# Kernel tuning notes

Hardware: AMD Instinct MI355X
Metric: run time of the kernel (lower is better)

## Reference

```python
import jax, jax.numpy as jnp
import numpy as np

B = 4096
D = 512
N_CLASSES = 100
TEMPERATURE = 0.5


def setup_inputs() -> dict:
    key = jax.random.key(0)
    k1, k2, k3 = jax.random.split(key, 3)
    emb_i = jax.random.normal(k1, (B, D), dtype=jnp.float32)
    emb_j = jax.random.normal(k2, (B, D), dtype=jnp.float32)
    target = jax.random.randint(k3, (B,), 0, N_CLASSES, dtype=jnp.int64)
    return {"emb_i": emb_i, "emb_j": emb_j, "target": target}


def _l2_normalize(x, eps=1e-12):
    # matches torch F.normalize(dim=1): x / max(||x||, eps)
    n = jnp.sqrt(jnp.sum(x * x, axis=1, keepdims=True))
    return x / jnp.maximum(n, eps)


def reference(emb_i, emb_j, target):
    size = emb_i.shape[0]          # B
    n2 = 2 * size                  # 2B
    t = jnp.float32(TEMPERATURE)

    z_i = _l2_normalize(emb_i)
    z_j = _l2_normalize(emb_j)
    reps = jnp.concatenate([z_i, z_j], axis=0)                 # [2B, D]
    sim = jnp.matmul(reps, reps.T)                             # [2B, 2B]

    # positives: diag at offsets +B and -B
    sim_ij = jnp.diagonal(sim, offset=size)                    # [B]
    sim_ji = jnp.diagonal(sim, offset=-size)                   # [B]
    positives = jnp.concatenate([sim_ij, sim_ji], axis=0)      # [2B]
    nominator = jnp.exp(positives / t)

    idx = jnp.arange(n2)
    labels = jnp.concatenate([target, target])                 # [2B]
    # sample_mask: zero where same label AND |i-j| != B (also zeros the diagonal)
    same_label = labels[:, None] == labels[None, :]
    not_pos_pair = jnp.abs(idx[:, None] - idx[None, :]) != size
    sample_mask = jnp.where(same_label & not_pos_pair, 0.0, 1.0).astype(jnp.float32)
    # negatives_mask: ~eye
    neg_mask = 1.0 - jnp.eye(n2, dtype=jnp.float32)

    denom = jnp.sum(sample_mask * neg_mask * jnp.exp(sim / t), axis=1)  # [2B]
    loss_partial = -jnp.log(nominator / (denom + 1e-7))
    loss = jnp.sum(loss_partial) / n2
    return loss
```

## Files before the change

kernel.cpp:

```cpp
#include <hip/hip_runtime.h>
#include <hip/hip_bf16.h>
#include <cstdint>

#define B_SIZE 4096
#define TWO_B  8192
#define DIM    512
#define NPAIRS 2080
#define EXP_SCALE 2.8853900817779268f

typedef __attribute__((ext_vector_type(4))) float f32x4;

#define WAITVM(n) __builtin_amdgcn_s_waitcnt(0xF70 | (n))
#define BARRIER() __builtin_amdgcn_s_barrier()

__device__ __forceinline__ void async16(const void* g, void* l) {
    __builtin_amdgcn_global_load_lds(
        (const __attribute__((address_space(1))) unsigned int*)g,
        (__attribute__((address_space(3))) unsigned int*)l,
        16, 0, 0);
}

__global__ __launch_bounds__(256) void norm_pos_kernel(
    const float* __restrict__ emb_i, const float* __restrict__ emb_j,
    unsigned char* __restrict__ reps, float* __restrict__ pos,
    float* __restrict__ denom, float* __restrict__ out)
{
    __shared__ float sc[3][4];
    int b = blockIdx.x, t = threadIdx.x;
    if (b < 32) denom[b * 256 + t] = 0.0f;
    if (b == 32 && t == 0) out[0] = 0.0f;

    const float2* ri = (const float2*)(emb_i + (size_t)b * DIM);
    const float2* rj = (const float2*)(emb_j + (size_t)b * DIM);
    float2 xi = ri[t], xj = rj[t];
    float si = xi.x * xi.x + xi.y * xi.y;
    float sj = xj.x * xj.x + xj.y * xj.y;
    #pragma unroll
    for (int o = 32; o > 0; o >>= 1) { si += __shfl_down(si, o, 64); sj += __shfl_down(sj, o, 64); }
    int lane = t & 63, w = t >> 6;
    if (lane == 0) { sc[0][w] = si; sc[1][w] = sj; }
    __syncthreads();
    float ni2 = sc[0][0] + sc[0][1] + sc[0][2] + sc[0][3];
    float nj2 = sc[1][0] + sc[1][1] + sc[1][2] + sc[1][3];
    float rni = 1.0f / fmaxf(sqrtf(ni2), 1e-12f);
    float rnj = 1.0f / fmaxf(sqrtf(nj2), 1e-12f);
    float zix = xi.x * rni, ziy = xi.y * rni;
    float zjx = xj.x * rnj, zjy = xj.y * rnj;
    int pki = __builtin_amdgcn_cvt_pk_fp8_f32(zix, ziy, 0, false);
    int pkj = __builtin_amdgcn_cvt_pk_fp8_f32(zjx, zjy, 0, false);
    ((unsigned short*)(reps + (size_t)b * DIM))[t]            = (unsigned short)pki;
    ((unsigned short*)(reps + (size_t)(b + B_SIZE) * DIM))[t] = (unsigned short)pkj;
    float d = zix * zjx + ziy * zjy;
    #pragma unroll
    for (int o = 32; o > 0; o >>= 1) d += __shfl_down(d, o, 64);
    if (lane == 0) sc[2][w] = d;
    __syncthreads();
    if (t == 0) pos[b] = sc[2][0] + sc[2][1] + sc[2][2] + sc[2][3];
}

#define BM 128
#define BK 64
#define KITERS 8

__global__ __launch_bounds__(256) void sim_denom_kernel(
    const unsigned char* __restrict__ reps,
    const int* __restrict__ target,
    float* __restrict__ denom)
{
    __shared__ __align__(16) unsigned char As0[BM * BK];
    __shared__ __align__(16) unsigned char As1[BM * BK];
    __shared__ __align__(16) unsigned char Bs0[BM * BK];
    __shared__ __align__(16) unsigned char Bs1[BM * BK];

    int t = threadIdx.x;
    int id = blockIdx.x;

    const int sI[10]  = {0,0,0,0,1,1,1,2,2,3};
    const int sJ[10]  = {0,1,2,3,1,2,3,2,3,3};
    const int off[11] = {0,136,392,648,904,1040,1296,1552,1688,1944,2080};
    int s = 0;
    while (off[s + 1] <= id) s++;
    int l = id - off[s];
    int u, v;
    if (sI[s] == sJ[s]) {
        u = 0;
        while (((u + 1) * (32 - u)) / 2 <= l) u++;
        v = u + (l - (u * (33 - u)) / 2);
    } else { u = l >> 4; v = l & 15; }
    int bi = sI[s] * 16 + u;
    int bj = sJ[s] * 16 + v;
    int brow = bi * BM;
    int bcol = bj * BM;

    int wave = t >> 6, lane = t & 63;
    int wr = wave >> 1, wc = wave & 1;
    int quad = lane >> 4, lm = lane & 15;

    f32x4 acc[4][4];
    #pragma unroll
    for (int i = 0; i < 4; i++)
        #pragma unroll
        for (int j = 0; j < 4; j++) acc[i][j] = (f32x4)0.0f;

    int srow = t >> 2;
    int sp   = (t & 3) ^ ((srow ^ (srow >> 2)) & 3);
    const unsigned char* gA = reps + (size_t)(brow + srow) * DIM + sp * 16;
    const unsigned char* gB = reps + (size_t)(bcol + srow) * DIM + sp * 16;

    auto stage = [&](unsigned char* Ab, unsigned char* Bb, int k0) {
        #pragma unroll
        for (int c = 0; c < 2; c++) {
            async16(gA + k0 + c * 64 * DIM, Ab + t * 16 + c * 4096);
            async16(gB + k0 + c * 64 * DIM, Bb + t * 16 + c * 4096);
        }
    };
    auto compute = [&](const unsigned char* Ab, const unsigned char* Bb) {
        #pragma unroll
        for (int ss = 0; ss < 2; ss++) {
            long af[4], bf[4];
            #pragma unroll
            for (int mi = 0; mi < 4; mi++) {
                int rl = wr * 64 + mi * 16 + lm;
                int p = (ss * 2 + (quad >> 1)) ^ ((rl ^ (rl >> 2)) & 3);
                af[mi] = *(const long*)(Ab + rl * 64 + p * 16 + (quad & 1) * 8);
            }
            #pragma unroll
            for (int ni = 0; ni < 4; ni++) {
                int cl = wc * 64 + ni * 16 + lm;
                int p = (ss * 2 + (quad >> 1)) ^ ((cl ^ (cl >> 2)) & 3);
                bf[ni] = *(const long*)(Bb + cl * 64 + p * 16 + (quad & 1) * 8);
            }
            #pragma unroll
            for (int mi = 0; mi < 4; mi++)
                #pragma unroll
                for (int ni = 0; ni < 4; ni++)
                    acc[mi][ni] = __builtin_amdgcn_mfma_f32_16x16x32_fp8_fp8(
                        af[mi], bf[ni], acc[mi][ni], 0, 0, 0);
        }
    };

    stage(As0, Bs0, 0);
    stage(As1, Bs1, BK);

    #pragma unroll
    for (int k = 0; k < KITERS; k++) {
        unsigned char* Ac = (k & 1) ? As1 : As0;
        unsigned char* Bc = (k & 1) ? Bs1 : Bs0;
        if (k < KITERS - 1) WAITVM(4); else WAITVM(0);
        BARRIER();
        compute(Ac, Bc);
        BARRIER();
        if (k + 2 < KITERS) stage(Ac, Bc, (k + 2) * BK);
    }

    bool haspos = (bj - bi == 32);
    int labc[4];
    #pragma unroll
    for (int ni = 0; ni < 4; ni++)
        labc[ni] = target[(bcol + wc * 64 + ni * 16 + lm) & (B_SIZE - 1)];

    float colacc[4] = {0.f, 0.f, 0.f, 0.f};
    #pragma unroll
    for (int mi = 0; mi < 4; mi++) {
        #pragma unroll
        for (int r = 0; r < 4; r++) {
            int rl = wr * 64 + mi * 16 + quad * 4 + r;
            int labr = target[(brow + rl) & (B_SIZE - 1)];
            float rowacc = 0.0f;
            #pragma unroll
            for (int ni = 0; ni < 4; ni++) {
                int cl = wc * 64 + ni * 16 + lm;
                bool pospair = haspos && (rl == cl);
                bool masked = (labr == labc[ni]) && !pospair;
                float e = masked ? 0.0f
                                 : __builtin_amdgcn_exp2f(acc[mi][ni][r] * EXP_SCALE);
                rowacc += e;
                colacc[ni] += e;
            }
            rowacc += __shfl_xor(rowacc, 1, 64);
            rowacc += __shfl_xor(rowacc, 2, 64);
            rowacc += __shfl_xor(rowacc, 4, 64);
            rowacc += __shfl_xor(rowacc, 8, 64);
            if (lm == 0) atomicAdd(&denom[brow + rl], rowacc);
        }
    }
    if (bi != bj) {
        #pragma unroll
        for (int ni = 0; ni < 4; ni++) {
            float c = colacc[ni];
            c += __shfl_xor(c, 16, 64);
            c += __shfl_xor(c, 32, 64);
            if (lane < 16) atomicAdd(&denom[bcol + wc * 64 + ni * 16 + lm], c);
        }
    }
}

__global__ __launch_bounds__(256) void loss_kernel(
    const float* __restrict__ denom, const float* __restrict__ pos,
    float* __restrict__ out)
{
    __shared__ float sc[4];
    int t = threadIdx.x, b = blockIdx.x;
    int i = b * 256 + t;
    float v = logf(denom[i] + 1e-7f);
    float p = (i < B_SIZE) ? pos[i] : 0.0f;
    float v2 = v - 4.0f * p;
    #pragma unroll
    for (int o = 32; o > 0; o >>= 1) v2 += __shfl_down(v2, o, 64);
    int lane = t & 63, w = t >> 6;
    if (lane == 0) sc[w] = v2;
    __syncthreads();
    if (t == 0) atomicAdd(out, (sc[0] + sc[1] + sc[2] + sc[3]) * (1.0f / (float)TWO_B));
}

extern "C" void kernel_launch(void* const* d_in, const int* in_sizes, int n_in,
                              void* d_out, int out_size, void* d_ws, size_t ws_size,
                              hipStream_t stream)
{
    const float* emb_i  = (const float*)d_in[0];
    const float* emb_j  = (const float*)d_in[1];
    const int*   target = (const int*)d_in[2];
    float* out = (float*)d_out;

    char* ws = (char*)d_ws;
    unsigned char* reps = (unsigned char*)ws;
    float* pos   = (float*)(ws + (size_t)TWO_B * DIM);
    float* denom = (float*)(ws + (size_t)TWO_B * DIM + B_SIZE * 4);

    norm_pos_kernel<<<B_SIZE, 256, 0, stream>>>(emb_i, emb_j, reps, pos, denom, out);
    sim_denom_kernel<<<NPAIRS, 256, 0, stream>>>(reps, target, denom);
    loss_kernel<<<TWO_B / 256, 256, 0, stream>>>(denom, pos, out);
}
```

Before: 122.8 us.

## Use 512-thread tiles, deterministic partial buffers instead of atomics, and block-id swizzle

Doubles the threads per 128x128 tile block to eight waves, so each wave holds a 64x32 accumulator. Row and column sums are reduced in shared memory and written to a per-tile-column partial buffer rather than atomically added to a global denominator. The loss kernel then sums 64 partials per row, which also removes the need to zero the denominator. Block IDs are remapped with a stride-260 interleave across the triangular tile schedule. This trades global atomics and register pressure for extra partial-buffer traffic and a 64-way read in the loss kernel.

```diff
diff --git a/kernel.cpp b/kernel.cpp
--- a/kernel.cpp
+++ b/kernel.cpp
@@ -23,12 +23,11 @@
 __global__ __launch_bounds__(256) void norm_pos_kernel(
     const float* __restrict__ emb_i, const float* __restrict__ emb_j,
     unsigned char* __restrict__ reps, float* __restrict__ pos,
-    float* __restrict__ denom, float* __restrict__ out)
+    float* __restrict__ out)
 {
     __shared__ float sc[3][4];
     int b = blockIdx.x, t = threadIdx.x;
-    if (b < 32) denom[b * 256 + t] = 0.0f;
-    if (b == 32 && t == 0) out[0] = 0.0f;
+    if (b == 0 && t == 0) out[0] = 0.0f;
 
     const float2* ri = (const float2*)(emb_i + (size_t)b * DIM);
     const float2* rj = (const float2*)(emb_j + (size_t)b * DIM);
@@ -62,10 +61,10 @@
 #define BK 64
 #define KITERS 8
 
-__global__ __launch_bounds__(256) void sim_denom_kernel(
+__global__ __launch_bounds__(512) void sim_denom_kernel(
     const unsigned char* __restrict__ reps,
     const int* __restrict__ target,
-    float* __restrict__ denom)
+    float* __restrict__ part)
 {
     __shared__ __align__(16) unsigned char As0[BM * BK];
     __shared__ __align__(16) unsigned char As1[BM * BK];
@@ -73,7 +72,8 @@
     __shared__ __align__(16) unsigned char Bs1[BM * BK];
 
     int t = threadIdx.x;
-    int id = blockIdx.x;
+    int id0 = blockIdx.x;
+    int id = (id0 & 7) * 260 + (id0 >> 3);
 
     const int sI[10]  = {0,0,0,0,1,1,1,2,2,3};
     const int sJ[10]  = {0,1,2,3,1,2,3,2,3,3};
@@ -93,14 +93,15 @@
     int bcol = bj * BM;
 
     int wave = t >> 6, lane = t & 63;
-    int wr = wave >> 1, wc = wave & 1;
+    int wr = wave >> 2, wc = wave & 3;
     int quad = lane >> 4, lm = lane & 15;
 
-    f32x4 acc[4][4];
-    #pragma unroll
-    for (int i = 0; i < 4; i++)
-        #pragma unroll
-        for (int j = 0; j < 4; j++) acc[i][j] = (f32x4)0.0f;
+    f32x4 acc[4][2];
+    #pragma unroll
+    for (int i = 0; i < 4; i++) {
+        acc[i][0] = (f32x4)0.0f;
+        acc[i][1] = (f32x4)0.0f;
+    }
 
     int srow = t >> 2;
     int sp   = (t & 3) ^ ((srow ^ (srow >> 2)) & 3);
@@ -108,16 +109,13 @@
     const unsigned char* gB = reps + (size_t)(bcol + srow) * DIM + sp * 16;
 
     auto stage = [&](unsigned char* Ab, unsigned char* Bb, int k0) {
-        #pragma unroll
-        for (int c = 0; c < 2; c++) {
-            async16(gA + k0 + c * 64 * DIM, Ab + t * 16 + c * 4096);
-            async16(gB + k0 + c * 64 * DIM, Bb + t * 16 + c * 4096);
-        }
+        async16(gA + k0, Ab + t * 16);
+        async16(gB + k0, Bb + t * 16);
     };
     auto compute = [&](const unsigned char* Ab, const unsigned char* Bb) {
         #pragma unroll
         for (int ss = 0; ss < 2; ss++) {
-            long af[4], bf[4];
+            long af[4], bf[2];
             #pragma unroll
             for (int mi = 0; mi < 4; mi++) {
                 int rl = wr * 64 + mi * 16 + lm;
@@ -125,15 +123,15 @@
                 af[mi] = *(const long*)(Ab + rl * 64 + p * 16 + (quad & 1) * 8);
             }
             #pragma unroll
-            for (int ni = 0; ni < 4; ni++) {
-                int cl = wc * 64 + ni * 16 + lm;
+            for (int ni = 0; ni < 2; ni++) {
+                int cl = wc * 32 + ni * 16 + lm;
                 int p = (ss * 2 + (quad >> 1)) ^ ((cl ^ (cl >> 2)) & 3);
                 bf[ni] = *(const long*)(Bb + cl * 64 + p * 16 + (quad & 1) * 8);
             }
             #pragma unroll
             for (int mi = 0; mi < 4; mi++)
                 #pragma unroll
-                for (int ni = 0; ni < 4; ni++)
+                for (int ni = 0; ni < 2; ni++)
                     acc[mi][ni] = __builtin_amdgcn_mfma_f32_16x16x32_fp8_fp8(
                         af[mi], bf[ni], acc[mi][ni], 0, 0, 0);
         }
@@ -146,7 +144,7 @@
     for (int k = 0; k < KITERS; k++) {
         unsigned char* Ac = (k & 1) ? As1 : As0;
         unsigned char* Bc = (k & 1) ? Bs1 : Bs0;
-        if (k < KITERS - 1) WAITVM(4); else WAITVM(0);
+        if (k < KITERS - 1) WAITVM(2); else WAITVM(0);
         BARRIER();
         compute(Ac, Bc);
         BARRIER();
@@ -154,12 +152,15 @@
     }
 
     bool haspos = (bj - bi == 32);
-    int labc[4];
-    #pragma unroll
-    for (int ni = 0; ni < 4; ni++)
-        labc[ni] = target[(bcol + wc * 64 + ni * 16 + lm) & (B_SIZE - 1)];
-
-    float colacc[4] = {0.f, 0.f, 0.f, 0.f};
+    int labc[2];
+    #pragma unroll
+    for (int ni = 0; ni < 2; ni++)
+        labc[ni] = target[(bcol + wc * 32 + ni * 16 + lm) & (B_SIZE - 1)];
+
+    float* red_row = (float*)As0;
+    float* red_col = (float*)Bs0;
+
+    float colacc[2] = {0.f, 0.f};
     #pragma unroll
     for (int mi = 0; mi < 4; mi++) {
         #pragma unroll
@@ -168,8 +169,8 @@
             int labr = target[(brow + rl) & (B_SIZE - 1)];
             float rowacc = 0.0f;
             #pragma unroll
-            for (int ni = 0; ni < 4; ni++) {
-                int cl = wc * 64 + ni * 16 + lm;
+            for (int ni = 0; ni < 2; ni++) {
+                int cl = wc * 32 + ni * 16 + lm;
                 bool pospair = haspos && (rl == cl);
                 bool masked = (labr == labc[ni]) && !pospair;
                 float e = masked ? 0.0f
@@ -181,28 +182,40 @@
             rowacc += __shfl_xor(rowacc, 2, 64);
             rowacc += __shfl_xor(rowacc, 4, 64);
             rowacc += __shfl_xor(rowacc, 8, 64);
-            if (lm == 0) atomicAdd(&denom[brow + rl], rowacc);
+            if (lm == 0) red_row[wc * 128 + rl] = rowacc;
         }
     }
-    if (bi != bj) {
-        #pragma unroll
-        for (int ni = 0; ni < 4; ni++) {
-            float c = colacc[ni];
-            c += __shfl_xor(c, 16, 64);
-            c += __shfl_xor(c, 32, 64);
-            if (lane < 16) atomicAdd(&denom[bcol + wc * 64 + ni * 16 + lm], c);
+    #pragma unroll
+    for (int ni = 0; ni < 2; ni++) {
+        float c = colacc[ni];
+        c += __shfl_xor(c, 16, 64);
+        c += __shfl_xor(c, 32, 64);
+        if (quad == 0) red_col[wr * 128 + wc * 32 + ni * 16 + lm] = c;
+    }
+    BARRIER();
+    if (t < 128) {
+        float rs = red_row[t] + red_row[128 + t] + red_row[256 + t] + red_row[384 + t];
+        part[(size_t)bj * TWO_B + brow + t] = rs;
+    } else if (t < 256) {
+        if (bi != bj) {
+            int c = t - 128;
+            float cs = red_col[c] + red_col[128 + c];
+            part[(size_t)bi * TWO_B + bcol + c] = cs;
         }
     }
 }
 
 __global__ __launch_bounds__(256) void loss_kernel(
-    const float* __restrict__ denom, const float* __restrict__ pos,
+    const float* __restrict__ part, const float* __restrict__ pos,
     float* __restrict__ out)
 {
     __shared__ float sc[4];
     int t = threadIdx.x, b = blockIdx.x;
     int i = b * 256 + t;
-    float v = logf(denom[i] + 1e-7f);
+    float s = 0.0f;
+    #pragma unroll
+    for (int x = 0; x < 64; x++) s += part[(size_t)x * TWO_B + i];
+    float v = logf(s + 1e-7f);
     float p = (i < B_SIZE) ? pos[i] : 0.0f;
     float v2 = v - 4.0f * p;
     #pragma unroll
@@ -225,9 +238,9 @@
     char* ws = (char*)d_ws;
     unsigned char* reps = (unsigned char*)ws;
     float* pos   = (float*)(ws + (size_t)TWO_B * DIM);
-    float* denom = (float*)(ws + (size_t)TWO_B * DIM + B_SIZE * 4);
-
-    norm_pos_kernel<<<B_SIZE, 256, 0, stream>>>(emb_i, emb_j, reps, pos, denom, out);
-    sim_denom_kernel<<<NPAIRS, 256, 0, stream>>>(reps, target, denom);
-    loss_kernel<<<TWO_B / 256, 256, 0, stream>>>(denom, pos, out);
-}
+    float* part  = (float*)(ws + (size_t)TWO_B * DIM + B_SIZE * 4);
+
+    norm_pos_kernel<<<B_SIZE, 256, 0, stream>>>(emb_i, emb_j, reps, pos, out);
+    sim_denom_kernel<<<NPAIRS, 512, 0, stream>>>(reps, target, part);
+    loss_kernel<<<TWO_B / 256, 256, 0, stream>>>(part, pos, out);
+}
```

New measurement: 120.7 us. No clear change (-1.7%).

## Use 256x128 tiles with 512 threads and deterministic partial-sum buffer instead of atomics

Applied to the files above, without the earlier changes.

The similarity kernel now uses 256x128 tiles with 8 waves, launched over 1056 blocks of the upper-triangular tile set, and a block index swizzle spreads work across XCDs. Row and column exp-sums are reduced in LDS and written to a per-column-tile partial buffer instead of being accumulated with global atomics. The loss kernel sums 64 partials per row, which replaces the denominator zeroing and the atomic contention. The cost is extra global traffic for the partial buffer and a longer reduction in the loss kernel.

```diff
diff --git a/kernel.cpp b/kernel.cpp
--- a/kernel.cpp
+++ b/kernel.cpp
@@ -5,7 +5,7 @@
 #define B_SIZE 4096
 #define TWO_B  8192
 #define DIM    512
-#define NPAIRS 2080
+#define NBLK   1056
 #define EXP_SCALE 2.8853900817779268f
 
 typedef __attribute__((ext_vector_type(4))) float f32x4;
@@ -23,12 +23,11 @@
 __global__ __launch_bounds__(256) void norm_pos_kernel(
     const float* __restrict__ emb_i, const float* __restrict__ emb_j,
     unsigned char* __restrict__ reps, float* __restrict__ pos,
-    float* __restrict__ denom, float* __restrict__ out)
+    float* __restrict__ out)
 {
     __shared__ float sc[3][4];
     int b = blockIdx.x, t = threadIdx.x;
-    if (b < 32) denom[b * 256 + t] = 0.0f;
-    if (b == 32 && t == 0) out[0] = 0.0f;
+    if (b == 0 && t == 0) out[0] = 0.0f;
 
     const float2* ri = (const float2*)(emb_i + (size_t)b * DIM);
     const float2* rj = (const float2*)(emb_j + (size_t)b * DIM);
@@ -58,39 +57,39 @@
     if (t == 0) pos[b] = sc[2][0] + sc[2][1] + sc[2][2] + sc[2][3];
 }
 
-#define BM 128
 #define BK 64
 #define KITERS 8
 
-__global__ __launch_bounds__(256) void sim_denom_kernel(
+__global__ __launch_bounds__(512) void sim_denom_kernel(
     const unsigned char* __restrict__ reps,
     const int* __restrict__ target,
-    float* __restrict__ denom)
-{
-    __shared__ __align__(16) unsigned char As0[BM * BK];
-    __shared__ __align__(16) unsigned char As1[BM * BK];
-    __shared__ __align__(16) unsigned char Bs0[BM * BK];
-    __shared__ __align__(16) unsigned char Bs1[BM * BK];
+    float* __restrict__ part)
+{
+    __shared__ __align__(16) unsigned char As0[256 * BK];
+    __shared__ __align__(16) unsigned char As1[256 * BK];
+    __shared__ __align__(16) unsigned char Bs0[128 * BK];
+    __shared__ __align__(16) unsigned char Bs1[128 * BK];
 
     int t = threadIdx.x;
-    int id = blockIdx.x;
-
-    const int sI[10]  = {0,0,0,0,1,1,1,2,2,3};
-    const int sJ[10]  = {0,1,2,3,1,2,3,2,3,3};
-    const int off[11] = {0,136,392,648,904,1040,1296,1552,1688,1944,2080};
+    int id0 = blockIdx.x;
+    int id = (id0 & 7) * 132 + (id0 >> 3);
+
+    const int bA[10]   = {0,0,0,0,1,1,1,2,2,3};
+    const int bB[10]   = {0,1,2,3,1,2,3,2,3,3};
+    const int boff[11] = {0,72,200,328,456,528,656,784,856,984,1056};
     int s = 0;
-    while (off[s + 1] <= id) s++;
-    int l = id - off[s];
-    int u, v;
-    if (sI[s] == sJ[s]) {
-        u = 0;
-        while (((u + 1) * (32 - u)) / 2 <= l) u++;
-        v = u + (l - (u * (33 - u)) / 2);
-    } else { u = l >> 4; v = l & 15; }
-    int bi = sI[s] * 16 + u;
-    int bj = sJ[s] * 16 + v;
-    int brow = bi * BM;
-    int bcol = bj * BM;
+    while (boff[s + 1] <= id) s++;
+    int l = id - boff[s];
+    int I, J;
+    if (bA[s] == bB[s]) {
+        int r = 0;
+        while ((r + 1) * (16 - r) <= l) r++;
+        I = bA[s] * 8 + r;
+        J = bB[s] * 16 + 2 * r + (l - r * (17 - r));
+    } else { I = bA[s] * 8 + (l >> 4); J = bB[s] * 16 + (l & 15); }
+
+    int brow = I * 256;
+    int bcol = J * 128;
 
     int wave = t >> 6, lane = t & 63;
     int wr = wave >> 1, wc = wave & 1;
@@ -108,11 +107,9 @@
     const unsigned char* gB = reps + (size_t)(bcol + srow) * DIM + sp * 16;
 
     auto stage = [&](unsigned char* Ab, unsigned char* Bb, int k0) {
-        #pragma unroll
-        for (int c = 0; c < 2; c++) {
-            async16(gA + k0 + c * 64 * DIM, Ab + t * 16 + c * 4096);
-            async16(gB + k0 + c * 64 * DIM, Bb + t * 16 + c * 4096);
-        }
+        async16(gA + k0, Ab + t * 16);
+        async16(gA + k0 + 128 * DIM, Ab + t * 16 + 8192);
+        async16(gB + k0, Bb + t * 16);
     };
     auto compute = [&](const unsigned char* Ab, const unsigned char* Bb) {
         #pragma unroll
@@ -146,18 +143,23 @@
     for (int k = 0; k < KITERS; k++) {
         unsigned char* Ac = (k & 1) ? As1 : As0;
         unsigned char* Bc = (k & 1) ? Bs1 : Bs0;
-        if (k < KITERS - 1) WAITVM(4); else WAITVM(0);
+        if (k < KITERS - 1) WAITVM(3); else WAITVM(0);
         BARRIER();
         compute(Ac, Bc);
         BARRIER();
         if (k + 2 < KITERS) stage(Ac, Bc, (k + 2) * BK);
     }
 
-    bool haspos = (bj - bi == 32);
+    int h = wr >> 1;
+    int rtile = 2 * I + h;
+    bool haspos = (J - rtile == 32);
     int labc[4];
     #pragma unroll
     for (int ni = 0; ni < 4; ni++)
         labc[ni] = target[(bcol + wc * 64 + ni * 16 + lm) & (B_SIZE - 1)];
+
+    float* red_row = (float*)As0;
+    float* red_col = (float*)Bs0;
 
     float colacc[4] = {0.f, 0.f, 0.f, 0.f};
     #pragma unroll
@@ -170,7 +172,7 @@
             #pragma unroll
             for (int ni = 0; ni < 4; ni++) {
                 int cl = wc * 64 + ni * 16 + lm;
-                bool pospair = haspos && (rl == cl);
+                bool pospair = haspos && ((rl & 127) == cl);
                 bool masked = (labr == labc[ni]) && !pospair;
                 float e = masked ? 0.0f
                                  : __builtin_amdgcn_exp2f(acc[mi][ni][r] * EXP_SCALE);
@@ -181,28 +183,45 @@
             rowacc += __shfl_xor(rowacc, 2, 64);
             rowacc += __shfl_xor(rowacc, 4, 64);
             rowacc += __shfl_xor(rowacc, 8, 64);
-            if (lm == 0) atomicAdd(&denom[brow + rl], rowacc);
-        }
-    }
-    if (bi != bj) {
-        #pragma unroll
-        for (int ni = 0; ni < 4; ni++) {
-            float c = colacc[ni];
-            c += __shfl_xor(c, 16, 64);
-            c += __shfl_xor(c, 32, 64);
-            if (lane < 16) atomicAdd(&denom[bcol + wc * 64 + ni * 16 + lm], c);
+            if (lm == 0) red_row[wc * 256 + rl] = rowacc;
+        }
+    }
+    #pragma unroll
+    for (int ni = 0; ni < 4; ni++) {
+        float c = colacc[ni];
+        c += __shfl_xor(c, 16, 64);
+        c += __shfl_xor(c, 32, 64);
+        if (quad == 0) red_col[h * 256 + (wr & 1) * 128 + wc * 64 + ni * 16 + lm] = c;
+    }
+    BARRIER();
+    if (t < 256) {
+        int th = t >> 7;
+        if (2 * I + th <= J) {
+            float rs = red_row[t] + red_row[256 + t];
+            part[(size_t)J * TWO_B + brow + t] = rs;
+        }
+    } else if (t < 512) {
+        int c = t - 256;
+        int ch = c >> 7, cc = c & 127;
+        int rt = 2 * I + ch;
+        if (rt < J) {
+            float cs = red_col[ch * 256 + cc] + red_col[ch * 256 + 128 + cc];
+            part[(size_t)rt * TWO_B + bcol + cc] = cs;
         }
     }
 }
 
 __global__ __launch_bounds__(256) void loss_kernel(
-    const float* __restrict__ denom, const float* __restrict__ pos,
+    const float* __restrict__ part, const float* __restrict__ pos,
     float* __restrict__ out)
 {
     __shared__ float sc[4];
     int t = threadIdx.x, b = blockIdx.x;
     int i = b * 256 + t;
-    float v = logf(denom[i] + 1e-7f);
+    float s = 0.0f;
+    #pragma unroll
+    for (int x = 0; x < 64; x++) s += part[(size_t)x * TWO_B + i];
+    float v = logf(s + 1e-7f);
     float p = (i < B_SIZE) ? pos[i] : 0.0f;
     float v2 = v - 4.0f * p;
     #pragma unroll
@@ -225,9 +244,9 @@
     char* ws = (char*)d_ws;
     unsigned char* reps = (unsigned char*)ws;
     float* pos   = (float*)(ws + (size_t)TWO_B * DIM);
-    float* denom = (float*)(ws + (size_t)TWO_B * DIM + B_SIZE * 4);
-
-    norm_pos_kernel<<<B_SIZE, 256, 0, stream>>>(emb_i, emb_j, reps, pos, denom, out);
-    sim_denom_kernel<<<NPAIRS, 256, 0, stream>>>(reps, target, denom);
-    loss_kernel<<<TWO_B / 256, 256, 0, stream>>>(denom, pos, out);
-}
+    float* part  = (float*)(ws + (size_t)TWO_B * DIM + B_SIZE * 4);
+
+    norm_pos_kernel<<<B_SIZE, 256, 0, stream>>>(emb_i, emb_j, reps, pos, out);
+    sim_denom_kernel<<<NBLK, 512, 0, stream>>>(reps, target, part);
+    loss_kernel<<<TWO_B / 256, 256, 0, stream>>>(part, pos, out);
+}
```

After: 131.7 us. 7.2% more time.
